# Optimization experiments

Hardware: AMD Instinct MI355X
Metric: run time of the kernel (lower is better)

The kernel has to match this reference:

```python
import jax, jax.numpy as jnp
import numpy as np

N, B, M, C, NH, S, HC, T, OUT = 8, 256, 512, 512, 8, 8, 64, 3, 100
DH = C // NH


def setup_inputs() -> dict:
    key = jax.random.key(0)
    it = iter(jax.random.split(key, 40))
    def nrm(shape, s=0.02):
        return jax.random.normal(next(it), shape, jnp.float32) * s
    z = lambda shape: jnp.zeros(shape, jnp.float32)
    return {
        "x": jax.random.normal(next(it), (B, 3, 32, 32), jnp.float32),
        "conv1_w": nrm((N, 64, 3, 3, 3)), "conv1_b": z((N, 64)),
        "conv2_w": nrm((N, 128, 64, 3, 3)), "conv2_b": z((N, 128)),
        "feat_w": nrm((N, 128, M)), "feat_b": z((N, M)),
        "ctrl_wi": nrm((N, M, 3 * HC)), "ctrl_wh": nrm((N, HC, 3 * HC)),
        "ctrl_bi": z((N, 3 * HC)), "ctrl_bh": z((N, 3 * HC)),
        "send_w": nrm((N, HC, 1)), "send_b": z((N, 1)),
        "recv_w": nrm((N, HC, 1)), "recv_b": z((N, 1)),
        "abias_w": nrm((N, HC, NH)), "abias_b": z((N, NH)),
        "wq": nrm((N, M, C)), "wk": nrm((N, M, C)), "wv": nrm((N, M, C)),
        "wo": nrm((N, C, C)), "bo": z((N, C)),
        "edge_logits": nrm((N, N), 0.1),
        "wr": nrm((N, C, M)), "br": z((N, M)),
        "wg": nrm((N, 3 * M, M)), "bg": z((N, M)),
        "wc": nrm((N, 3 * M, M)), "bc": z((N, M)),
        "wcls": nrm((N, M, OUT)), "bcls": z((N, OUT)),
    }


def _forward(x, conv1_w, conv1_b, conv2_w, conv2_b, feat_w, feat_b,
             ctrl_wi, ctrl_wh, ctrl_bi, ctrl_bh,
             send_w, send_b, recv_w, recv_b, abias_w, abias_b,
             wq, wk, wv, wo, bo, edge_logits, wr, br,
             wg, bg, wc, bc, wcls, bcls):
    dn = ('NCHW', 'OIHW', 'NCHW')
    def conv(inp, w, b):
        y = jax.lax.conv_general_dilated(inp, w, (2, 2), 'SAME', dimension_numbers=dn)
        return jax.nn.relu(y + b[None, :, None, None])
    # per-node feature extraction (batched over N experts via vmap)
    h1 = jax.vmap(lambda w, b: conv(x, w, b))(conv1_w, conv1_b)          # [N,B,64,16,16]
    h2 = jax.vmap(conv, in_axes=(0, 0, 0))(h1, conv2_w, conv2_b)        # [N,B,128,8,8]
    pooled = h2.mean(axis=(-2, -1))                                      # [N,B,128]
    feats = jax.nn.relu(jnp.einsum('nbf,nfm->nbm', pooled, feat_w) + feat_b[:, None, :])
    h = feats                                                            # node states [N,B,M]
    cs = jnp.zeros((N, B, HC), x.dtype)                                  # controller GRU states
    buf = jnp.zeros((N, B, S, C), x.dtype)                               # message buffers
    scale = 1.0 / jnp.sqrt(jnp.asarray(DH, x.dtype))
    for t in range(T):
        # controller (GRUCell) -> send/recv gates + per-head attention bias
        gi = jnp.einsum('nbm,nmh->nbh', h, ctrl_wi) + ctrl_bi[:, None, :]
        gh = jnp.einsum('nbh,nhk->nbk', cs, ctrl_wh) + ctrl_bh[:, None, :]
        iz, ir, inn = jnp.split(gi, 3, -1)
        hz, hr, hn = jnp.split(gh, 3, -1)
        zg = jax.nn.sigmoid(iz + hz)
        rg = jax.nn.sigmoid(ir + hr)
        ng = jnp.tanh(inn + rg * hn)
        cs = (1.0 - zg) * ng + zg * cs
        send = jax.nn.sigmoid(jnp.einsum('nbh,nho->nbo', cs, send_w) + send_b[:, None, :])  # [N,B,1]
        recv = jax.nn.sigmoid(jnp.einsum('nbh,nho->nbo', cs, recv_w) + recv_b[:, None, :])  # [N,B,1]
        ab = jnp.einsum('nbh,nhk->nbk', cs, abias_w) + abias_b[:, None, :]                  # [N,B,NH]
        # per-node QKV
        q = jnp.einsum('nbm,nmc->nbc', h, wq).reshape(N, B, NH, DH)
        k = jnp.einsum('nbm,nmc->nbc', h, wk).reshape(N, B, NH, DH)
        v = jnp.einsum('nbm,nmc->nbc', h, wv).reshape(N, B, NH, DH)
        # graph-transformer attention over nodes: i=receiver, j=sender
        scores = jnp.einsum('ibhd,jbhd->ijbh', q, k) * scale
        scores = scores + edge_logits[:, :, None, None] + ab[:, None, :, :]
        attn = jax.nn.softmax(scores, axis=1)
        attn = attn * send[None, :, :, :] * recv[:, None, :, :]          # gated [N,N,B,NH]
        msg = jnp.einsum('ijbh,jbhd->ibhd', attn, v).reshape(N, B, C)
        msg = jnp.einsum('nbc,nck->nbk', msg, wo) + bo[:, None, :]
        # push into FIFO buffer, read out mean
        buf = jnp.concatenate([buf[:, :, 1:], msg[:, :, None, :]], axis=2)
        readout = jnp.einsum('nbc,ncm->nbm', buf.mean(axis=2), wr) + br[:, None, :]
        # gated state update fusing h, fresh features, buffer readout
        cat = jnp.concatenate([h, feats, readout], axis=-1)              # [N,B,3M]
        g = jax.nn.sigmoid(jnp.einsum('nbk,nkm->nbm', cat, wg) + bg[:, None, :])
        cand = jnp.tanh(jnp.einsum('nbk,nkm->nbm', cat, wc) + bc[:, None, :])
        h = (1.0 - g) * h + g * cand
    logits = jnp.einsum('nbm,nmo->nbo', h, wcls) + bcls[:, None, :]      # [N,B,OUT]
    return logits


def reference(x, conv1_w, conv1_b, conv2_w, conv2_b, feat_w, feat_b,
              ctrl_wi, ctrl_wh, ctrl_bi, ctrl_bh,
              send_w, send_b, recv_w, recv_b, abias_w, abias_b,
              wq, wk, wv, wo, bo, edge_logits, wr, br,
              wg, bg, wc, bc, wcls, bcls):
    return _forward(x, conv1_w, conv1_b, conv2_w, conv2_b, feat_w, feat_b,
                    ctrl_wi, ctrl_wh, ctrl_bi, ctrl_bh,
                    send_w, send_b, recv_w, recv_b, abias_w, abias_b,
                    wq, wk, wv, wo, bo, edge_logits, wr, br,
                    wg, bg, wc, bc, wcls, bcls)
```

## Files before the change

### kernel.cpp

```cpp
#include <hip/hip_runtime.h>
#include <hip/hip_bf16.h>


typedef _Float16 f16;
typedef _Float16 f16x8 __attribute__((ext_vector_type(8)));
typedef _Float16 f16x4 __attribute__((ext_vector_type(4)));
typedef _Float16 f16x2 __attribute__((ext_vector_type(2)));
typedef float f32x4 __attribute__((ext_vector_type(4)));

#define GLOAD_LDS16(gsrc, ldst)                                                   \
  __builtin_amdgcn_global_load_lds(                                               \
      (const __attribute__((address_space(1))) void*)(gsrc),                      \
      (__attribute__((address_space(3))) void*)(ldst), 16, 0, 0)

__device__ __forceinline__ void tw64_body(
    const float* __restrict__ s, f16* __restrict__ d, int K, int N, float scale,
    int n0, int k0, int t)
{
  __shared__ float tile[64][65];
#pragma unroll
  for (int p = 0; p < 4; p++) {
    int idx = t + p * 256;
    int kk = idx >> 4, nq = (idx & 15) * 4;
    float4 v = *(const float4*)&s[(long)(k0 + kk) * N + n0 + nq];
    tile[kk][nq] = v.x; tile[kk][nq + 1] = v.y; tile[kk][nq + 2] = v.z; tile[kk][nq + 3] = v.w;
  }
  __syncthreads();
#pragma unroll
  for (int p = 0; p < 2; p++) {
    int idx = t + p * 256;
    int nn = idx >> 3, kc = (idx & 7) * 8;
    f16 o[8];
#pragma unroll
    for (int i = 0; i < 8; i++) o[i] = (f16)(tile[kc + i][nn] * scale);
    *(f16x8*)&d[(long)(n0 + nn) * K + k0 + kc] = *(const f16x8*)o;
  }
}

__global__ __launch_bounds__(256) void twmulti6_kernel(
    const float* __restrict__ wq, const float* __restrict__ wk,
    const float* __restrict__ wv, const float* __restrict__ wi,
    const float* __restrict__ wr, const float* __restrict__ fw,
    f16* __restrict__ wqT, f16* __restrict__ wiT,
    f16* __restrict__ wrT, f16* __restrict__ featwT)
{
  int z = blockIdx.z, sel = z >> 3, e = z & 7;
  int n0 = blockIdx.x * 64, k0 = blockIdx.y * 64;
  const float* src;
  f16* dst;
  int K = 512, N = 512;
  float scale = 1.f;
  if (sel == 0)      { src = wq + (long)e * 262144; dst = wqT + (long)e * 262144; }
  else if (sel == 1) { src = wk + (long)e * 262144; dst = wqT + 2097152 + (long)e * 262144; }
  else if (sel == 2) { src = wv + (long)e * 262144; dst = wqT + 4194304 + (long)e * 262144; }
  else if (sel == 3) {
    N = 192; if (n0 >= 192) return;
    src = wi + (long)e * 98304; dst = wiT + (long)e * 98304;
  } else if (sel == 4) {
    scale = 0.125f;
    src = wr + (long)e * 262144; dst = wrT + (long)e * 262144;
  } else {
    K = 128; if (k0 >= 128) return;
    src = fw + (long)e * 65536; dst = featwT + (long)e * 65536;
  }
  tw64_body(src, dst, K, N, scale, n0, k0, threadIdx.x);
}

__global__ __launch_bounds__(256) void twmulti2_kernel(
    const float* __restrict__ wg, const float* __restrict__ wc, f16* __restrict__ wgT)
{
  int z = blockIdx.z, sel = z >> 3, e = z & 7;
  const float* src = sel ? wc : wg;
  f16* dst = wgT + (long)sel * 6291456 + (long)e * 786432;
  tw64_body(src + (long)e * 786432, dst, 1536, 512, 1.f,
            blockIdx.x * 64, blockIdx.y * 64, threadIdx.x);
}

__global__ __launch_bounds__(256) void smallprep_kernel(
    const float* __restrict__ wo, f16* __restrict__ wo16,
    const float* __restrict__ c2src, f16* __restrict__ c2dst,
    const float* __restrict__ w1src, f16* __restrict__ w1dst,
    const float* __restrict__ wcls, f16* __restrict__ wclsT)
{
  __shared__ float tile[32][33];
  int bid = blockIdx.x, t = threadIdx.x;
  if (bid < 1024) {
    long i = ((long)bid * 256 + t) * 8;
    float4 a = *(const float4*)&wo[i];
    float4 b = *(const float4*)&wo[i + 4];
    f16 o[8] = {(f16)a.x, (f16)a.y, (f16)a.z, (f16)a.w, (f16)b.x, (f16)b.y, (f16)b.z, (f16)b.w};
    *(f16x8*)&wo16[i] = *(const f16x8*)o;
  } else if (bid < 3328) {
    long i = (long)(bid - 1024) * 256 + t;
    int ci = i & 63; long r = i >> 6; int tap = r % 9; r /= 9; int co = r & 127; int n = (int)(r >> 7);
    c2dst[i] = (f16)c2src[(((long)(n * 128 + co) * 64 + ci) * 9) + tap];
  } else if (bid < 3392) {
    int i = (bid - 3328) * 256 + t;
    int j = i & 7, co = (i >> 3) & 63, slot = (i >> 9) & 3, e = i >> 11;
    int k = slot * 8 + j;
    w1dst[i] = (f16)((k < 27) ? w1src[(long)e * 1728 + co * 27 + k] : 0.f);
  } else {
    int bid2 = bid - 3392;
    int e = bid2 >> 6, ky = (bid2 >> 2) & 15, nx = bid2 & 3;
    int n0 = nx * 32, k0 = ky * 32;
    int tx = t & 31, ty = t >> 5;
    const float* s = wcls + (long)e * 51200;
    f16* d = wclsT + (long)e * 65536;
    for (int r = ty; r < 32; r += 8) {
      int k = k0 + r, n = n0 + tx;
      tile[r][tx] = (n < 100) ? s[(long)k * 100 + n] : 0.f;
    }
    __syncthreads();
    for (int r = ty; r < 32; r += 8) {
      int n = n0 + r, k = k0 + tx;
      d[(long)n * 512 + k] = (f16)tile[tx][r];
    }
  }
}

__global__ __launch_bounds__(256) void xprep_kernel(
    const float* __restrict__ x, f16* __restrict__ xp16)
{
  __shared__ float xs[3072];
  int b = blockIdx.x, t = threadIdx.x;
  const float* xb = x + (long)b * 3072;
  for (int i = t; i < 768; i += 256) ((float4*)xs)[i] = ((const float4*)xb)[i];
  __syncthreads();
  int oy = t >> 4, ox = t & 15;
  f16 pv[32];
#pragma unroll
  for (int q = 27; q < 32; q++) pv[q] = (f16)0.f;
#pragma unroll
  for (int ci = 0; ci < 3; ci++)
#pragma unroll
    for (int ky = 0; ky < 3; ky++) {
      int iy = oy * 2 + ky;
#pragma unroll
      for (int kx = 0; kx < 3; kx++) {
        int ix = ox * 2 + kx;
        pv[ci * 9 + ky * 3 + kx] =
            (f16)((iy < 32 && ix < 32) ? xs[ci * 1024 + iy * 32 + ix] : 0.f);
      }
    }
  f16* ob = xp16 + (long)b * 8192;
#pragma unroll
  for (int c = 0; c < 4; c++) *(f16x8*)&ob[c * 2048 + t * 8] = *(const f16x8*)&pv[c * 8];
}

__global__ __launch_bounds__(256) void borprep2_kernel(
    const f16* __restrict__ wrT, const float* __restrict__ bo, float* __restrict__ bor32)
{
  int n = blockIdx.y, t = threadIdx.x;
  int og = blockIdx.x * 16 + (t >> 4), k16 = t & 15;
  const f16* row = wrT + (long)n * 262144 + (long)og * 512 + k16 * 32;
  const float* bp = bo + n * 512 + k16 * 32;
  float s = 0.f;
#pragma unroll
  for (int i = 0; i < 32; i += 8) {
    f16x8 v = *(const f16x8*)&row[i];
    float4 b0 = *(const float4*)&bp[i];
    float4 b1 = *(const float4*)&bp[i + 4];
    s = fmaf((float)v[0], b0.x, s); s = fmaf((float)v[1], b0.y, s);
    s = fmaf((float)v[2], b0.z, s); s = fmaf((float)v[3], b0.w, s);
    s = fmaf((float)v[4], b1.x, s); s = fmaf((float)v[5], b1.y, s);
    s = fmaf((float)v[6], b1.z, s); s = fmaf((float)v[7], b1.w, s);
  }
  s += __shfl_xor(s, 1); s += __shfl_xor(s, 2);
  s += __shfl_xor(s, 4); s += __shfl_xor(s, 8);
  if (k16 == 0) bor32[n * 512 + og] = s;
}

__global__ __launch_bounds__(256) void biasfold2_kernel(
    const f16* __restrict__ wgT, const f16* __restrict__ wcT,
    const float* __restrict__ bg, const float* __restrict__ bc,
    const float* __restrict__ br, const float* __restrict__ bor32,
    float* __restrict__ bgr, float* __restrict__ vg2,
    float* __restrict__ bcr, float* __restrict__ vc2)
{
  int n = blockIdx.y, t = threadIdx.x;
  int og = blockIdx.x * 16 + (t >> 4), k16 = t & 15;
  const f16* gr = wgT + (long)n * 786432 + (long)og * 1536 + 1024 + k16 * 32;
  const f16* cr = wcT + (long)n * 786432 + (long)og * 1536 + 1024 + k16 * 32;
  const float* brp = br + n * 512 + k16 * 32;
  const float* bop = bor32 + n * 512 + k16 * 32;
  float s1g = 0.f, s2g = 0.f, s1c = 0.f, s2c = 0.f;
#pragma unroll
  for (int i = 0; i < 32; i += 8) {
    f16x8 gv = *(const f16x8*)&gr[i];
    f16x8 cv = *(const f16x8*)&cr[i];
#pragma unroll
    for (int q = 0; q < 8; q++) {
      float brm = brp[i + q], bom = bop[i + q];
      s1g = fmaf(brm, (float)gv[q], s1g); s2g = fmaf(bom, (float)gv[q], s2g);
      s1c = fmaf(brm, (float)cv[q], s1c); s2c = fmaf(bom, (float)cv[q], s2c);
    }
  }
#pragma unroll
  for (int o = 1; o < 16; o <<= 1) {
    s1g += __shfl_xor(s1g, o); s2g += __shfl_xor(s2g, o);
    s1c += __shfl_xor(s1c, o); s2c += __shfl_xor(s2c, o);
  }
  if (k16 == 0) {
    bgr[n * 512 + og] = bg[n * 512 + og] + s1g; vg2[n * 512 + og] = s2g;
    bcr[n * 512 + og] = bc[n * 512 + og] + s1c; vc2[n * 512 + og] = s2c;
  }
}

__global__ __launch_bounds__(256) void convfused_kernel(
    const f16* __restrict__ xp16, const f16* __restrict__ w1p, const float* __restrict__ b1,
    const f16* __restrict__ w2p, const float* __restrict__ b2, f16* __restrict__ pooled16)
{
  __shared__ __align__(16) char lds[53632];
  f16* xpatch = (f16*)lds;
  f16* AsubS = (f16*)lds;
  float* red = (float*)lds;
  float* bs1 = (float*)(lds + 16384);
  f16* h1s = (f16*)(lds + 16640);
  f16* ws1 = (f16*)(lds + 16640);

  int b = blockIdx.x, e = blockIdx.y;
  int t = threadIdx.x, w = t >> 6, l = t & 63;

  const f16* xb = xp16 + (long)b * 8192;
#pragma unroll
  for (int c = 0; c < 4; c++)
    GLOAD_LDS16(xb + (w * 4 + c) * 512 + l * 8, &xpatch[(w * 4 + c) * 512]);
  GLOAD_LDS16(w1p + (long)e * 2048 + w * 512 + l * 8, &ws1[w * 512]);
  if (t < 64) bs1[t] = b1[e * 64 + t];
  asm volatile("s_waitcnt vmcnt(0)" ::: "memory");
  __syncthreads();

  {
    int pw = w * 64;
    f16x8 a1[4], b1f[4];
#pragma unroll
    for (int i = 0; i < 4; i++)
      a1[i] = *(const f16x8*)&ws1[(l >> 4) * 512 + (i * 16 + (l & 15)) * 8];
#pragma unroll
    for (int jj = 0; jj < 4; jj++)
      b1f[jj] = *(const f16x8*)&xpatch[(l >> 4) * 2048 + (pw + jj * 16 + (l & 15)) * 8];
    __syncthreads();
    f32x4 acc1[4][4];
#pragma unroll
    for (int i = 0; i < 4; i++)
#pragma unroll
      for (int jj = 0; jj < 4; jj++)
        acc1[i][jj] = __builtin_amdgcn_mfma_f32_16x16x32_f16(
            a1[i], b1f[jj], (f32x4){0.f, 0.f, 0.f, 0.f}, 0, 0, 0);
#pragma unroll
    for (int i = 0; i < 4; i++) {
      int co0 = i * 16 + ((l >> 4) << 2);
      float bi0 = bs1[co0], bi1 = bs1[co0 + 1], bi2 = bs1[co0 + 2], bi3 = bs1[co0 + 3];
#pragma unroll
      for (int jj = 0; jj < 4; jj++) {
        int p2 = pw + jj * 16 + (l & 15);
        int oy2 = p2 >> 4, ox2 = p2 & 15;
        int p = oy2 * 17 + ox2;
        int fs = ((ox2 >> 1) + oy2) & 7;
        int slot = (co0 >> 3) ^ fs;
        f16x4 v;
        v[0] = (f16)fmaxf(acc1[i][jj][0] + bi0, 0.f);
        v[1] = (f16)fmaxf(acc1[i][jj][1] + bi1, 0.f);
        v[2] = (f16)fmaxf(acc1[i][jj][2] + bi2, 0.f);
        v[3] = (f16)fmaxf(acc1[i][jj][3] + bi3, 0.f);
        *(f16x4*)&h1s[p * 64 + slot * 8 + (co0 & 7)] = v;
      }
    }
  }
  if (t < 33) {
    int gy = (t < 17) ? 16 : (t - 17);
    int gx = (t < 17) ? t : 16;
    int p = gy * 17 + gx;
    f16x8 zz = {};
#pragma unroll
    for (int g = 0; g < 8; g++) *(f16x8*)&h1s[p * 64 + g * 8] = zz;
  }

  int waveR = w >> 1, waveC = w & 1;
  const f16* wbase = w2p + (long)e * 73728;
  f32x4 acc[4][2];
#pragma unroll
  for (int i = 0; i < 4; i++) {
    acc[i][0] = (f32x4){0.f, 0.f, 0.f, 0.f};
    acc[i][1] = (f32x4){0.f, 0.f, 0.f, 0.f};
  }
  for (int tap = 0; tap < 9; tap++) {
    __syncthreads();
#pragma unroll
    for (int c = 0; c < 4; c++) {
      int ch = w * 4 + c;
      int co = ch * 8 + (l >> 3);
      int g = (l & 7) ^ (co & 7);
      GLOAD_LDS16(wbase + ((long)co * 9 + tap) * 64 + g * 8, &AsubS[ch * 512]);
    }
    asm volatile("s_waitcnt vmcnt(0)" ::: "memory");
    __syncthreads();
    int ky = tap / 3, kx = tap - ky * 3;
#pragma unroll
    for (int kk = 0; kk < 2; kk++) {
      f16x8 af[4], bf[2];
#pragma unroll
      for (int i = 0; i < 4; i++) {
        int row = waveR * 64 + i * 16 + (l & 15);
        int blk = (kk * 4 + (l >> 4)) ^ (row & 7);
        af[i] = *(const f16x8*)&AsubS[row * 64 + blk * 8];
      }
#pragma unroll
      for (int j = 0; j < 2; j++) {
        int sp = waveC * 32 + j * 16 + (l & 15);
        int iy = (sp >> 3) * 2 + ky, ix = (sp & 7) * 2 + kx;
        int fs = ((ix >> 1) + iy) & 7;
        int blk = (kk * 4 + (l >> 4)) ^ fs;
        bf[j] = *(const f16x8*)&h1s[(iy * 17 + ix) * 64 + blk * 8];
      }
#pragma unroll
      for (int i = 0; i < 4; i++)
#pragma unroll
        for (int j = 0; j < 2; j++)
          acc[i][j] = __builtin_amdgcn_mfma_f32_16x16x32_f16(af[i], bf[j], acc[i][j], 0, 0, 0);
    }
  }
  __syncthreads();
  const float* bn2 = b2 + e * 128;
#pragma unroll
  for (int i = 0; i < 4; i++) {
#pragma unroll
    for (int reg = 0; reg < 4; reg++) {
      int row = waveR * 64 + i * 16 + ((l >> 4) << 2) + reg;
      float bi = bn2[row];
      float s = fmaxf(acc[i][0][reg] + bi, 0.f) + fmaxf(acc[i][1][reg] + bi, 0.f);
      s += __shfl_xor(s, 1); s += __shfl_xor(s, 2);
      s += __shfl_xor(s, 4); s += __shfl_xor(s, 8);
      if ((l & 15) == 0) red[waveC * 128 + row] = s;
    }
  }
  __syncthreads();
  if (t < 128) {
    float v = (red[t] + red[128 + t]) * (1.f / 64.f);
    pooled16[((long)e * 256 + b) * 128 + t] = (f16)v;
  }
}

struct SegsM {
  const f16* BT[4];
  const float* bias[4];
  f16* o16[4];
  f16* o16b[4];
  float* o32[4];
  long sBT[4], sBias[4], sO16[4], sO32[4];
  int ldo16[4], ldo32[4], act[4], segCols[4];
};

template <int MR>
__global__ __launch_bounds__(256) void gemmf16_kernel(
    const f16* __restrict__ A, long sA, int lda, SegsM segs, int K)
{
  constexpr int IW = MR / 32;
  __shared__ __align__(16) f16 Asub[2][MR * 64];
  __shared__ __align__(16) f16 Bsub[2][4096];
  int z = blockIdx.z;
  int rowBase = blockIdx.y * MR;
  int vcBase = blockIdx.x * 64;
  int seg = vcBase >> 9;
  int lcBase = vcBase & 511;
  const f16* An = A + (long)z * sA + (long)rowBase * lda;
  const f16* BTn = segs.BT[seg] + (long)z * segs.sBT[seg] + (long)lcBase * K;
  const float* biasN = segs.bias[seg] ? segs.bias[seg] + (long)z * segs.sBias[seg] : nullptr;
  int act = segs.act[seg];
  int segCols = segs.segCols[seg];
  int t = threadIdx.x, w = t >> 6, l = t & 63;
  int waveR = w >> 1, waveC = w & 1;
  f32x4 acc[IW][2];
#pragma unroll
  for (int i = 0; i < IW; i++) {
    acc[i][0] = (f32x4){0.f, 0.f, 0.f, 0.f};
    acc[i][1] = (f32x4){0.f, 0.f, 0.f, 0.f};
  }
  auto stage = [&](int buf, int kt) {
    int k0 = kt << 6;
#pragma unroll
    for (int c = 0; c < MR / 32; c++) {
      int ch = w * (MR / 32) + c;
      int row = ch * 8 + (l >> 3);
      int g = (l & 7) ^ (row & 7);
      GLOAD_LDS16(An + (long)row * lda + k0 + g * 8, &Asub[buf][ch * 512]);
    }
#pragma unroll
    for (int c = 0; c < 2; c++) {
      int ch = w * 2 + c;
      int col = ch * 8 + (l >> 3);
      int g = (l & 7) ^ (col & 7);
      GLOAD_LDS16(BTn + (long)col * K + k0 + g * 8, &Bsub[buf][ch * 512]);
    }
  };
  int nk = K >> 6;
  stage(0, 0);
  asm volatile("s_waitcnt vmcnt(0)" ::: "memory");
  __syncthreads();
  int cur = 0;
  for (int kt = 0; kt < nk; kt++) {
    if (kt + 1 < nk) stage(cur ^ 1, kt + 1);
#pragma unroll
    for (int kk = 0; kk < 2; kk++) {
      f16x8 af[IW], bf[2];
#pragma unroll
      for (int i = 0; i < IW; i++) {
        int row = waveR * (MR / 2) + i * 16 + (l & 15);
        int blk = (kk * 4 + (l >> 4)) ^ (row & 7);
        af[i] = *(const f16x8*)&Asub[cur][row * 64 + blk * 8];
      }
#pragma unroll
      for (int j = 0; j < 2; j++) {
        int col = waveC * 32 + j * 16 + (l & 15);
        int blk = (kk * 4 + (l >> 4)) ^ (col & 7);
        bf[j] = *(const f16x8*)&Bsub[cur][col * 64 + blk * 8];
      }
#pragma unroll
      for (int i = 0; i < IW; i++)
#pragma unroll
        for (int j = 0; j < 2; j++)
          acc[i][j] = __builtin_amdgcn_mfma_f32_16x16x32_f16(af[i], bf[j], acc[i][j], 0, 0, 0);
    }
    if (kt + 1 < nk) {
      asm volatile("s_waitcnt vmcnt(0)" ::: "memory");
      __syncthreads();
      cur ^= 1;
    }
  }
  f16* o16 = segs.o16[seg];
  f16* o16b = segs.o16b[seg];
  float* o32 = segs.o32[seg];
  long sO16 = segs.sO16[seg], sO32 = segs.sO32[seg];
  int ldo16 = segs.ldo16[seg], ldo32 = segs.ldo32[seg];
#pragma unroll
  for (int i = 0; i < IW; i++) {
    int rb = rowBase + waveR * (MR / 2) + i * 16 + ((l >> 4) << 2);
#pragma unroll
    for (int j = 0; j < 2; j++) {
      int lc = lcBase + waveC * 32 + j * 16 + (l & 15);
      if (lc >= segCols) continue;
      float bv = biasN ? biasN[lc] : 0.f;
#pragma unroll
      for (int reg = 0; reg < 4; reg++) {
        float v = acc[i][j][reg] + bv;
        if (act == 1) v = fmaxf(v, 0.f);
        else if (act == 2) v = 1.f / (1.f + __expf(-v));
        else if (act == 3) v = tanhf(v);
        long rr = rb + reg;
        if (o16) o16[(long)z * sO16 + rr * ldo16 + lc] = (f16)v;
        if (o16b) o16b[(long)z * sO16 + rr * ldo16 + lc] = (f16)v;
        if (o32) o32[(long)z * sO32 + rr * ldo32 + lc] = v;
      }
    }
  }
}

__global__ __launch_bounds__(256) void step_kernel(
    const f16* __restrict__ qkv16, const float* __restrict__ gi32,
    const float* __restrict__ wh, const float* __restrict__ bh,
    float* __restrict__ cs, const float* __restrict__ sw, const float* __restrict__ sb,
    const float* __restrict__ rw, const float* __restrict__ rb,
    const float* __restrict__ aw, const float* __restrict__ abb,
    const float* __restrict__ edge,
    float* __restrict__ msgsum32, f16* __restrict__ msgsum16, int step)
{
  int b = blockIdx.x, t = threadIdx.x;
  __shared__ float qs[8 * 520], ks[8 * 520];
  __shared__ f16 vs16[8 * 520];
  __shared__ float csh[512];
  __shared__ float sc[512];
  __shared__ float se[8], re[8], edg[64], abl[64];

  for (int i = t; i < 2048; i += 256) {
    int nn = i >> 8, c2 = (i & 255) * 2;
    int h = c2 >> 6, d = c2 & 63;
    long base = ((long)nn * 256 + b) * 1536 + c2;
    int la = nn * 520 + h * 65 + d;
    f16x2 qv = *(const f16x2*)&qkv16[base];
    f16x2 kv = *(const f16x2*)&qkv16[base + 512];
    *(f16x2*)&vs16[la] = *(const f16x2*)&qkv16[base + 1024];
    qs[la] = (float)qv[0]; qs[la + 1] = (float)qv[1];
    ks[la] = (float)kv[0]; ks[la + 1] = (float)kv[1];
  }
  if (t >= 192) edg[t - 192] = edge[t - 192];
  int n0 = t >> 6, hc = t & 63;
  if (step > 0) {
    csh[t] = cs[((long)n0 * 256 + b) * 64 + hc];
    csh[t + 256] = cs[((long)(n0 + 4) * 256 + b) * 64 + hc];
  }
  __syncthreads();

  float cn[2];
#pragma unroll
  for (int u = 0; u < 2; u++) {
    int n = n0 + u * 4;
    long nb = (long)n * 256 + b;
    float c0 = (step > 0) ? csh[n * 64 + hc] : 0.f;
    float g0 = bh[n * 192 + hc], g1 = bh[n * 192 + 64 + hc], g2 = bh[n * 192 + 128 + hc];
    if (step > 0) {
      const float* whn = wh + (long)n * 12288;
      for (int k = 0; k < 64; k++) {
        float cv = csh[n * 64 + k];
        g0 = fmaf(cv, whn[k * 192 + hc], g0);
        g1 = fmaf(cv, whn[k * 192 + 64 + hc], g1);
        g2 = fmaf(cv, whn[k * 192 + 128 + hc], g2);
      }
    }
    const float* gi = gi32 + nb * 192;
    float zg = 1.f / (1.f + __expf(-(gi[hc] + g0)));
    float rg = 1.f / (1.f + __expf(-(gi[64 + hc] + g1)));
    float ng = tanhf(gi[128 + hc] + rg * g2);
    cn[u] = (1.f - zg) * ng + zg * c0;
    cs[nb * 64 + hc] = cn[u];
  }
#pragma unroll
  for (int u = 0; u < 2; u++) {
    int n = n0 + u * 4;
    float ps = cn[u] * sw[n * 64 + hc];
    float pr = cn[u] * rw[n * 64 + hc];
#pragma unroll
    for (int o = 32; o; o >>= 1) { ps += __shfl_xor(ps, o); pr += __shfl_xor(pr, o); }
    if (hc == 0) {
      se[n] = 1.f / (1.f + __expf(-(ps + sb[n])));
      re[n] = 1.f / (1.f + __expf(-(pr + rb[n])));
    }
#pragma unroll
    for (int kk = 0; kk < 8; kk++) {
      float pa = cn[u] * aw[(n * 64 + hc) * 8 + kk];
#pragma unroll
      for (int o = 32; o; o >>= 1) pa += __shfl_xor(pa, o);
      if (hc == 0) abl[n * 8 + kk] = pa + abb[n * 8 + kk];
    }
  }
  __syncthreads();

  for (int idx = t; idx < 512; idx += 256) {
    int i = idx >> 6, j = (idx >> 3) & 7, h = idx & 7;
    const float* qp = &qs[i * 520 + h * 65];
    const float* kp = &ks[j * 520 + h * 65];
    float s = 0.f;
#pragma unroll
    for (int d = 0; d < 64; d++) s = fmaf(qp[d], kp[d], s);
    sc[idx] = s * 0.125f + edg[i * 8 + j] + abl[i * 8 + h];
  }
  __syncthreads();
  if (t < 64) {
    int i = t >> 3, h = t & 7;
    float mx = -1e30f;
#pragma unroll
    for (int j = 0; j < 8; j++) mx = fmaxf(mx, sc[(i << 6) + (j << 3) + h]);
    float e[8], sm = 0.f;
#pragma unroll
    for (int j = 0; j < 8; j++) { e[j] = __expf(sc[(i << 6) + (j << 3) + h] - mx); sm += e[j]; }
    float inv = re[i] / sm;
#pragma unroll
    for (int j = 0; j < 8; j++) sc[(i << 6) + (j << 3) + h] = e[j] * inv * se[j];
  }
  __syncthreads();
  for (int idx = t; idx < 4096; idx += 256) {
    int i = idx >> 9, c = idx & 511, h = c >> 6, d = c & 63;
    float s = 0.f;
#pragma unroll
    for (int j = 0; j < 8; j++)
      s = fmaf(sc[(i << 6) + (j << 3) + h], (float)vs16[j * 520 + h * 65 + d], s);
    long oi = ((long)i * 256 + b) * 512 + c;
    float nv = (step == 0) ? s : (msgsum32[oi] + s);
    msgsum32[oi] = nv;
    msgsum16[oi] = (f16)nv;
  }
}

__global__ __launch_bounds__(256) void gatefused_kernel(
    const f16* __restrict__ h16cur, const f16* __restrict__ feats16,
    const f16* __restrict__ msgsum16,
    const f16* __restrict__ wgT, const f16* __restrict__ wcT,
    const f16* __restrict__ WeffGT, const f16* __restrict__ WeffCT,
    const float* __restrict__ bgr, const float* __restrict__ vg2,
    const float* __restrict__ bcr, const float* __restrict__ vc2,
    float* __restrict__ h32, f16* __restrict__ h16next, float tp1)
{
  __shared__ __align__(16) f16 Asub[2][2048];
  __shared__ __align__(16) f16 Bgs[2][4096];
  __shared__ __align__(16) f16 Bcs[2][4096];
  int z = blockIdx.z;
  int rowBase = blockIdx.y * 32;
  int colBase = blockIdx.x * 64;
  int t = threadIdx.x, w = t >> 6, l = t & 63;
  int waveR = w >> 1, waveC = w & 1;
  f32x4 accG[2], accC[2];
  accG[0] = (f32x4){0.f, 0.f, 0.f, 0.f}; accG[1] = accG[0];
  accC[0] = accG[0]; accC[1] = accG[0];

  auto stage = [&](int buf, int kt) {
    {
      const f16* asrc;
      if (kt < 8)       asrc = h16cur  + (long)z * 131072 + kt * 64;
      else if (kt < 16) asrc = feats16 + (long)z * 131072 + (kt - 8) * 64;
      else              asrc = msgsum16 + (long)z * 131072 + (kt - 16) * 64;
      int row = w * 8 + (l >> 3);
      int g = (l & 7) ^ (row & 7);
      GLOAD_LDS16(asrc + (long)(rowBase + row) * 512 + g * 8, &Asub[buf][w * 512]);
    }
#pragma unroll
    for (int c = 0; c < 2; c++) {
      int ch = w * 2 + c;
      int cl = ch * 8 + (l >> 3);
      int g = (l & 7) ^ (cl & 7);
      const f16 *bgsrc, *bcsrc;
      if (kt < 16) {
        bgsrc = wgT + (long)z * 786432 + (long)(colBase + cl) * 1536 + kt * 64 + g * 8;
        bcsrc = wcT + (long)z * 786432 + (long)(colBase + cl) * 1536 + kt * 64 + g * 8;
      } else {
        bgsrc = WeffGT + (long)z * 262144 + (long)(colBase + cl) * 512 + (kt - 16) * 64 + g * 8;
        bcsrc = WeffCT + (long)z * 262144 + (long)(colBase + cl) * 512 + (kt - 16) * 64 + g * 8;
      }
      GLOAD_LDS16(bgsrc, &Bgs[buf][ch * 512]);
      GLOAD_LDS16(bcsrc, &Bcs[buf][ch * 512]);
    }
  };
  stage(0, 0);
  asm volatile("s_waitcnt vmcnt(0)" ::: "memory");
  __syncthreads();
  int cur = 0;
  for (int kt = 0; kt < 24; kt++) {
    if (kt + 1 < 24) stage(cur ^ 1, kt + 1);
#pragma unroll
    for (int kk = 0; kk < 2; kk++) {
      f16x8 af, bgf[2], bcf[2];
      {
        int row = waveR * 16 + (l & 15);
        int blk = (kk * 4 + (l >> 4)) ^ (row & 7);
        af = *(const f16x8*)&Asub[cur][row * 64 + blk * 8];
      }
#pragma unroll
      for (int j = 0; j < 2; j++) {
        int cl = waveC * 32 + j * 16 + (l & 15);
        int blk = (kk * 4 + (l >> 4)) ^ (cl & 7);
        bgf[j] = *(const f16x8*)&Bgs[cur][cl * 64 + blk * 8];
        bcf[j] = *(const f16x8*)&Bcs[cur][cl * 64 + blk * 8];
      }
#pragma unroll
      for (int j = 0; j < 2; j++) {
        accG[j] = __builtin_amdgcn_mfma_f32_16x16x32_f16(af, bgf[j], accG[j], 0, 0, 0);
        accC[j] = __builtin_amdgcn_mfma_f32_16x16x32_f16(af, bcf[j], accC[j], 0, 0, 0);
      }
    }
    if (kt + 1 < 24) {
      asm volatile("s_waitcnt vmcnt(0)" ::: "memory");
      __syncthreads();
      cur ^= 1;
    }
  }
#pragma unroll
  for (int j = 0; j < 2; j++) {
    int col = colBase + waveC * 32 + j * 16 + (l & 15);
    float bG = bgr[z * 512 + col] + tp1 * vg2[z * 512 + col];
    float bC = bcr[z * 512 + col] + tp1 * vc2[z * 512 + col];
#pragma unroll
    for (int reg = 0; reg < 4; reg++) {
      int row = rowBase + waveR * 16 + ((l >> 4) << 2) + reg;
      float g = 1.f / (1.f + __expf(-(accG[j][reg] + bG)));
      float cd = tanhf(accC[j][reg] + bC);
      long hidx = ((long)z * 256 + row) * 512 + col;
      float h = h32[hidx];
      float nh = (1.f - g) * h + g * cd;
      h32[hidx] = nh;
      h16next[hidx] = (f16)nh;
    }
  }
}

extern "C" void kernel_launch(void* const* d_in, const int* in_sizes, int n_in,
                              void* d_out, int out_size, void* d_ws, size_t ws_size,
                              hipStream_t stream)
{
  (void)in_sizes; (void)n_in; (void)out_size;
  const float* x        = (const float*)d_in[0];
  const float* conv1_w  = (const float*)d_in[1];
  const float* conv1_b  = (const float*)d_in[2];
  const float* conv2_w  = (const float*)d_in[3];
  const float* conv2_b  = (const float*)d_in[4];
  const float* feat_w   = (const float*)d_in[5];
  const float* feat_b   = (const float*)d_in[6];
  const float* ctrl_wi  = (const float*)d_in[7];
  const float* ctrl_wh  = (const float*)d_in[8];
  const float* ctrl_bi  = (const float*)d_in[9];
  const float* ctrl_bh  = (const float*)d_in[10];
  const float* send_w   = (const float*)d_in[11];
  const float* send_b   = (const float*)d_in[12];
  const float* recv_w   = (const float*)d_in[13];
  const float* recv_b   = (const float*)d_in[14];
  const float* abias_w  = (const float*)d_in[15];
  const float* abias_b  = (const float*)d_in[16];
  const float* wq       = (const float*)d_in[17];
  const float* wk       = (const float*)d_in[18];
  const float* wv       = (const float*)d_in[19];
  const float* wo       = (const float*)d_in[20];
  const float* bo       = (const float*)d_in[21];
  const float* edge     = (const float*)d_in[22];
  const float* wr       = (const float*)d_in[23];
  const float* br       = (const float*)d_in[24];
  const float* wg       = (const float*)d_in[25];
  const float* bg       = (const float*)d_in[26];
  const float* wc       = (const float*)d_in[27];
  const float* bc       = (const float*)d_in[28];
  const float* wcls     = (const float*)d_in[29];
  const float* bcls     = (const float*)d_in[30];

  float* f32b = (float*)d_ws;
  float* h32      = f32b;
  float* gi32     = f32b + 1048576;
  float* msgsum32 = f32b + 1441792;
  float* cs       = f32b + 2490368;
  float* bor32    = f32b + 2621440;
  float* bgr      = f32b + 2625536;
  float* vg2b     = f32b + 2629632;
  float* bcr      = f32b + 2633728;
  float* vc2b     = f32b + 2637824;
  f16* hb = (f16*)(f32b + 2641920);
  f16* pooled16 = hb;
  f16* h16a     = hb + 262144;
  f16* h16b     = hb + 1310720;
  f16* feats16  = hb + 2359296;
  f16* msgsum16 = hb + 3407872;
  f16* qkv16    = hb + 4456448;
  f16* wqT      = hb + 7602176;
  f16* wiT      = hb + 13893632;
  f16* featwT   = hb + 14680064;
  f16* wrT      = hb + 15204352;
  f16* wgT      = hb + 17301504;
  f16* wcT      = hb + 23592960;
  f16* c2wp     = hb + 29884416;
  f16* wo16     = hb + 30474240;
  f16* P        = hb + 32571392;
  f16* P2       = hb + 34668544;
  f16* WeffGT   = hb + 36765696;
  f16* WeffCT   = hb + 38862848;
  f16* w1p      = hb + 40960000;
  f16* xp16     = hb + 40976384;
  f16* wclsT    = hb + 43073536;
  if (ws_size < 97763328ull) return;

  f16* hbuf[2] = {h16a, h16b};

  twmulti6_kernel<<<dim3(8, 8, 48), 256, 0, stream>>>(
      wq, wk, wv, ctrl_wi, wr, feat_w, wqT, wiT, wrT, featwT);
  twmulti2_kernel<<<dim3(8, 24, 16), 256, 0, stream>>>(wg, wc, wgT);
  smallprep_kernel<<<3904, 256, 0, stream>>>(wo, wo16, conv2_w, c2wp, conv1_w, w1p,
                                             wcls, wclsT);
  xprep_kernel<<<256, 256, 0, stream>>>(x, xp16);
  borprep2_kernel<<<dim3(32, 8), 256, 0, stream>>>(wrT, bo, bor32);
  biasfold2_kernel<<<dim3(32, 8), 256, 0, stream>>>(wgT, wcT, bg, bc, br, bor32,
                                                    bgr, vg2b, bcr, vc2b);
  {
    SegsM s{};
    s.BT[0] = wrT; s.sBT[0] = 262144;
    s.o16[0] = P; s.o16b[0] = P2; s.sO16[0] = 262144; s.ldo16[0] = 512;
    s.segCols[0] = 512;
    gemmf16_kernel<64><<<dim3(8, 8, 8), 256, 0, stream>>>(wo16, 262144L, 512, s, 512);
  }
  {
    SegsM s{};
    s.BT[0] = P; s.sBT[0] = 262144;
    s.o16[0] = WeffGT; s.sO16[0] = 262144; s.ldo16[0] = 512;
    s.segCols[0] = 512;
    gemmf16_kernel<64><<<dim3(8, 8, 16), 256, 0, stream>>>(wgT + 1024, 786432L, 1536, s, 512);
  }

  convfused_kernel<<<dim3(256, 8), 256, 0, stream>>>(xp16, w1p, conv1_b, c2wp, conv2_b, pooled16);

  {
    SegsM s{};
    s.BT[0] = featwT; s.sBT[0] = 65536; s.bias[0] = feat_b; s.sBias[0] = 512; s.act[0] = 1;
    s.o16[0] = feats16; s.o16b[0] = h16a; s.sO16[0] = 131072; s.ldo16[0] = 512;
    s.o32[0] = h32; s.sO32[0] = 131072; s.ldo32[0] = 512;
    s.segCols[0] = 512;
    gemmf16_kernel<128><<<dim3(8, 2, 8), 256, 0, stream>>>(pooled16, 32768L, 128, s, 128);
  }

  for (int step = 0; step < 3; step++) {
    {
      SegsM s{};
      s.BT[0] = wqT;            s.sBT[0] = 262144;
      s.BT[1] = wqT + 2097152;  s.sBT[1] = 262144;
      s.BT[2] = wqT + 4194304;  s.sBT[2] = 262144;
      s.BT[3] = wiT;            s.sBT[3] = 98304;
      s.bias[3] = ctrl_bi; s.sBias[3] = 192;
      s.o16[0] = qkv16;        s.sO16[0] = 393216; s.ldo16[0] = 1536;
      s.o16[1] = qkv16 + 512;  s.sO16[1] = 393216; s.ldo16[1] = 1536;
      s.o16[2] = qkv16 + 1024; s.sO16[2] = 393216; s.ldo16[2] = 1536;
      s.o32[3] = gi32; s.sO32[3] = 49152; s.ldo32[3] = 192;
      s.segCols[0] = 512; s.segCols[1] = 512; s.segCols[2] = 512; s.segCols[3] = 192;
      gemmf16_kernel<128><<<dim3(27, 2, 8), 256, 0, stream>>>(hbuf[step & 1], 131072L, 512, s, 512);
    }
    step_kernel<<<256, 256, 0, stream>>>(
        qkv16, gi32, ctrl_wh, ctrl_bh, cs, send_w, send_b, recv_w, recv_b,
        abias_w, abias_b, edge, msgsum32, msgsum16, step);
    gatefused_kernel<<<dim3(8, 8, 8), 256, 0, stream>>>(
        hbuf[step & 1], feats16, msgsum16, wgT, wcT, WeffGT, WeffCT,
        bgr, vg2b, bcr, vc2b, h32, hbuf[(step + 1) & 1], (float)(step + 1));
  }
  {
    SegsM s{};
    s.BT[0] = wclsT; s.sBT[0] = 65536;
    s.bias[0] = bcls; s.sBias[0] = 100;
    s.o32[0] = (float*)d_out; s.sO32[0] = 25600; s.ldo32[0] = 100;
    s.segCols[0] = 100;
    gemmf16_kernel<128><<<dim3(2, 2, 8), 256, 0, stream>>>(hbuf[1], 131072L, 512, s, 512);
  }
}
```

Baseline: 321.3 us.

## Widen step kernel to 512 threads and enlarge gatefused row tile to 64

The step kernel now runs 512 threads per block, so each thread handles one expert's controller GRU column instead of looping over two, which halves the serial 64-step recurrent matvec per thread. The gate-fused GEMM kernel doubles its row tile from 32 to 64, so each wave computes a 2x2 grid of MFMA tiles and B-operand loads are reused across twice as many rows. The gate grid shrinks from 512 to 256 blocks, which trades parallelism and some occupancy (more LDS and accumulator registers) for less redundant weight traffic.

```diff
diff --git a/kernel.cpp b/kernel.cpp
--- a/kernel.cpp
+++ b/kernel.cpp
@@ -455,7 +455,7 @@
   }
 }
 
-__global__ __launch_bounds__(256) void step_kernel(
+__global__ __launch_bounds__(512) void step_kernel(
     const f16* __restrict__ qkv16, const float* __restrict__ gi32,
     const float* __restrict__ wh, const float* __restrict__ bh,
     float* __restrict__ cs, const float* __restrict__ sw, const float* __restrict__ sb,
@@ -471,7 +471,7 @@
   __shared__ float sc[512];
   __shared__ float se[8], re[8], edg[64], abl[64];
 
-  for (int i = t; i < 2048; i += 256) {
+  for (int i = t; i < 2048; i += 512) {
     int nn = i >> 8, c2 = (i & 255) * 2;
     int h = c2 >> 6, d = c2 & 63;
     long base = ((long)nn * 256 + b) * 1536 + c2;
@@ -482,42 +482,31 @@
     qs[la] = (float)qv[0]; qs[la + 1] = (float)qv[1];
     ks[la] = (float)kv[0]; ks[la + 1] = (float)kv[1];
   }
-  if (t >= 192) edg[t - 192] = edge[t - 192];
-  int n0 = t >> 6, hc = t & 63;
+  if (t >= 448) edg[t - 448] = edge[t - 448];
+  int n = t >> 6, hc = t & 63;
+  if (step > 0) csh[t] = cs[((long)n * 256 + b) * 64 + hc];
+  __syncthreads();
+
+  float c0 = (step > 0) ? csh[t] : 0.f;
+  float g0 = bh[n * 192 + hc], g1 = bh[n * 192 + 64 + hc], g2 = bh[n * 192 + 128 + hc];
   if (step > 0) {
-    csh[t] = cs[((long)n0 * 256 + b) * 64 + hc];
-    csh[t + 256] = cs[((long)(n0 + 4) * 256 + b) * 64 + hc];
-  }
-  __syncthreads();
-
-  float cn[2];
-#pragma unroll
-  for (int u = 0; u < 2; u++) {
-    int n = n0 + u * 4;
-    long nb = (long)n * 256 + b;
-    float c0 = (step > 0) ? csh[n * 64 + hc] : 0.f;
-    float g0 = bh[n * 192 + hc], g1 = bh[n * 192 + 64 + hc], g2 = bh[n * 192 + 128 + hc];
-    if (step > 0) {
-      const float* whn = wh + (long)n * 12288;
-      for (int k = 0; k < 64; k++) {
-        float cv = csh[n * 64 + k];
-        g0 = fmaf(cv, whn[k * 192 + hc], g0);
-        g1 = fmaf(cv, whn[k * 192 + 64 + hc], g1);
-        g2 = fmaf(cv, whn[k * 192 + 128 + hc], g2);
-      }
-    }
-    const float* gi = gi32 + nb * 192;
-    float zg = 1.f / (1.f + __expf(-(gi[hc] + g0)));
-    float rg = 1.f / (1.f + __expf(-(gi[64 + hc] + g1)));
-    float ng = tanhf(gi[128 + hc] + rg * g2);
-    cn[u] = (1.f - zg) * ng + zg * c0;
-    cs[nb * 64 + hc] = cn[u];
-  }
-#pragma unroll
-  for (int u = 0; u < 2; u++) {
-    int n = n0 + u * 4;
-    float ps = cn[u] * sw[n * 64 + hc];
-    float pr = cn[u] * rw[n * 64 + hc];
+    const float* whn = wh + (long)n * 12288;
+    for (int k = 0; k < 64; k++) {
+      float cv = csh[n * 64 + k];
+      g0 = fmaf(cv, whn[k * 192 + hc], g0);
+      g1 = fmaf(cv, whn[k * 192 + 64 + hc], g1);
+      g2 = fmaf(cv, whn[k * 192 + 128 + hc], g2);
+    }
+  }
+  const float* gi = gi32 + ((long)n * 256 + b) * 192;
+  float zg = 1.f / (1.f + __expf(-(gi[hc] + g0)));
+  float rg = 1.f / (1.f + __expf(-(gi[64 + hc] + g1)));
+  float ng = tanhf(gi[128 + hc] + rg * g2);
+  float cn = (1.f - zg) * ng + zg * c0;
+  cs[((long)n * 256 + b) * 64 + hc] = cn;
+  {
+    float ps = cn * sw[n * 64 + hc];
+    float pr = cn * rw[n * 64 + hc];
 #pragma unroll
     for (int o = 32; o; o >>= 1) { ps += __shfl_xor(ps, o); pr += __shfl_xor(pr, o); }
     if (hc == 0) {
@@ -526,7 +515,7 @@
     }
 #pragma unroll
     for (int kk = 0; kk < 8; kk++) {
-      float pa = cn[u] * aw[(n * 64 + hc) * 8 + kk];
+      float pa = cn * aw[(n * 64 + hc) * 8 + kk];
 #pragma unroll
       for (int o = 32; o; o >>= 1) pa += __shfl_xor(pa, o);
       if (hc == 0) abl[n * 8 + kk] = pa + abb[n * 8 + kk];
@@ -534,14 +523,14 @@
   }
   __syncthreads();
 
-  for (int idx = t; idx < 512; idx += 256) {
-    int i = idx >> 6, j = (idx >> 3) & 7, h = idx & 7;
+  {
+    int i = t >> 6, j = (t >> 3) & 7, h = t & 7;
     const float* qp = &qs[i * 520 + h * 65];
     const float* kp = &ks[j * 520 + h * 65];
     float s = 0.f;
 #pragma unroll
     for (int d = 0; d < 64; d++) s = fmaf(qp[d], kp[d], s);
-    sc[idx] = s * 0.125f + edg[i * 8 + j] + abl[i * 8 + h];
+    sc[t] = s * 0.125f + edg[i * 8 + j] + abl[i * 8 + h];
   }
   __syncthreads();
   if (t < 64) {
@@ -557,7 +546,7 @@
     for (int j = 0; j < 8; j++) sc[(i << 6) + (j << 3) + h] = e[j] * inv * se[j];
   }
   __syncthreads();
-  for (int idx = t; idx < 4096; idx += 256) {
+  for (int idx = t; idx < 4096; idx += 512) {
     int i = idx >> 9, c = idx & 511, h = c >> 6, d = c & 63;
     float s = 0.f;
 #pragma unroll
@@ -579,27 +568,34 @@
     const float* __restrict__ bcr, const float* __restrict__ vc2,
     float* __restrict__ h32, f16* __restrict__ h16next, float tp1)
 {
-  __shared__ __align__(16) f16 Asub[2][2048];
+  __shared__ __align__(16) f16 Asub[2][4096];
   __shared__ __align__(16) f16 Bgs[2][4096];
   __shared__ __align__(16) f16 Bcs[2][4096];
   int z = blockIdx.z;
-  int rowBase = blockIdx.y * 32;
+  int rowBase = blockIdx.y * 64;
   int colBase = blockIdx.x * 64;
   int t = threadIdx.x, w = t >> 6, l = t & 63;
   int waveR = w >> 1, waveC = w & 1;
-  f32x4 accG[2], accC[2];
-  accG[0] = (f32x4){0.f, 0.f, 0.f, 0.f}; accG[1] = accG[0];
-  accC[0] = accG[0]; accC[1] = accG[0];
+  f32x4 accG[2][2], accC[2][2];
+#pragma unroll
+  for (int i = 0; i < 2; i++)
+#pragma unroll
+    for (int j = 0; j < 2; j++) {
+      accG[i][j] = (f32x4){0.f, 0.f, 0.f, 0.f};
+      accC[i][j] = (f32x4){0.f, 0.f, 0.f, 0.f};
+    }
 
   auto stage = [&](int buf, int kt) {
-    {
-      const f16* asrc;
-      if (kt < 8)       asrc = h16cur  + (long)z * 131072 + kt * 64;
-      else if (kt < 16) asrc = feats16 + (long)z * 131072 + (kt - 8) * 64;
-      else              asrc = msgsum16 + (long)z * 131072 + (kt - 16) * 64;
-      int row = w * 8 + (l >> 3);
+    const f16* asrc;
+    if (kt < 8)       asrc = h16cur  + (long)z * 131072 + kt * 64;
+    else if (kt < 16) asrc = feats16 + (long)z * 131072 + (kt - 8) * 64;
+    else              asrc = msgsum16 + (long)z * 131072 + (kt - 16) * 64;
+#pragma unroll
+    for (int c = 0; c < 2; c++) {
+      int ch = w * 2 + c;
+      int row = ch * 8 + (l >> 3);
       int g = (l & 7) ^ (row & 7);
-      GLOAD_LDS16(asrc + (long)(rowBase + row) * 512 + g * 8, &Asub[buf][w * 512]);
+      GLOAD_LDS16(asrc + (long)(rowBase + row) * 512 + g * 8, &Asub[buf][ch * 512]);
     }
 #pragma unroll
     for (int c = 0; c < 2; c++) {
@@ -626,11 +622,12 @@
     if (kt + 1 < 24) stage(cur ^ 1, kt + 1);
 #pragma unroll
     for (int kk = 0; kk < 2; kk++) {
-      f16x8 af, bgf[2], bcf[2];
-      {
-        int row = waveR * 16 + (l & 15);
+      f16x8 af[2], bgf[2], bcf[2];
+#pragma unroll
+      for (int i = 0; i < 2; i++) {
+        int row = waveR * 32 + i * 16 + (l & 15);
         int blk = (kk * 4 + (l >> 4)) ^ (row & 7);
-        af = *(const f16x8*)&Asub[cur][row * 64 + blk * 8];
+        af[i] = *(const f16x8*)&Asub[cur][row * 64 + blk * 8];
       }
 #pragma unroll
       for (int j = 0; j < 2; j++) {
@@ -640,10 +637,12 @@
         bcf[j] = *(const f16x8*)&Bcs[cur][cl * 64 + blk * 8];
       }
 #pragma unroll
-      for (int j = 0; j < 2; j++) {
-        accG[j] = __builtin_amdgcn_mfma_f32_16x16x32_f16(af, bgf[j], accG[j], 0, 0, 0);
-        accC[j] = __builtin_amdgcn_mfma_f32_16x16x32_f16(af, bcf[j], accC[j], 0, 0, 0);
-      }
+      for (int i = 0; i < 2; i++)
+#pragma unroll
+        for (int j = 0; j < 2; j++) {
+          accG[i][j] = __builtin_amdgcn_mfma_f32_16x16x32_f16(af[i], bgf[j], accG[i][j], 0, 0, 0);
+          accC[i][j] = __builtin_amdgcn_mfma_f32_16x16x32_f16(af[i], bcf[j], accC[i][j], 0, 0, 0);
+        }
     }
     if (kt + 1 < 24) {
       asm volatile("s_waitcnt vmcnt(0)" ::: "memory");
@@ -652,20 +651,24 @@
     }
   }
 #pragma unroll
-  for (int j = 0; j < 2; j++) {
-    int col = colBase + waveC * 32 + j * 16 + (l & 15);
-    float bG = bgr[z * 512 + col] + tp1 * vg2[z * 512 + col];
-    float bC = bcr[z * 512 + col] + tp1 * vc2[z * 512 + col];
-#pragma unroll
-    for (int reg = 0; reg < 4; reg++) {
-      int row = rowBase + waveR * 16 + ((l >> 4) << 2) + reg;
-      float g = 1.f / (1.f + __expf(-(accG[j][reg] + bG)));
-      float cd = tanhf(accC[j][reg] + bC);
-      long hidx = ((long)z * 256 + row) * 512 + col;
-      float h = h32[hidx];
-      float nh = (1.f - g) * h + g * cd;
-      h32[hidx] = nh;
-      h16next[hidx] = (f16)nh;
+  for (int i = 0; i < 2; i++) {
+    int rb = rowBase + waveR * 32 + i * 16 + ((l >> 4) << 2);
+#pragma unroll
+    for (int j = 0; j < 2; j++) {
+      int col = colBase + waveC * 32 + j * 16 + (l & 15);
+      float bG = bgr[z * 512 + col] + tp1 * vg2[z * 512 + col];
+      float bC = bcr[z * 512 + col] + tp1 * vc2[z * 512 + col];
+#pragma unroll
+      for (int reg = 0; reg < 4; reg++) {
+        int row = rb + reg;
+        float g = 1.f / (1.f + __expf(-(accG[i][j][reg] + bG)));
+        float cd = tanhf(accC[i][j][reg] + bC);
+        long hidx = ((long)z * 256 + row) * 512 + col;
+        float h = h32[hidx];
+        float nh = (1.f - g) * h + g * cd;
+        h32[hidx] = nh;
+        h16next[hidx] = (f16)nh;
+      }
     }
   }
 }
@@ -793,10 +796,10 @@
       s.segCols[0] = 512; s.segCols[1] = 512; s.segCols[2] = 512; s.segCols[3] = 192;
       gemmf16_kernel<128><<<dim3(27, 2, 8), 256, 0, stream>>>(hbuf[step & 1], 131072L, 512, s, 512);
     }
-    step_kernel<<<256, 256, 0, stream>>>(
+    step_kernel<<<256, 512, 0, stream>>>(
         qkv16, gi32, ctrl_wh, ctrl_bh, cs, send_w, send_b, recv_w, recv_b,
         abias_w, abias_b, edge, msgsum32, msgsum16, step);
-    gatefused_kernel<<<dim3(8, 8, 8), 256, 0, stream>>>(
+    gatefused_kernel<<<dim3(8, 4, 8), 256, 0, stream>>>(
         hbuf[step & 1], feats16, msgsum16, wgT, wcT, WeffGT, WeffCT,
         bgr, vg2b, bcr, vc2b, h32, hbuf[(step + 1) & 1], (float)(step + 1));
   }
```

New measurement: 305.8 us. -4.8%, faster.
